# Optimization experiments

Hardware: AMD Instinct MI355X
Metric: run time of the kernel (lower is better)

The kernel has to match this reference:

```python
import jax, jax.numpy as jnp
import numpy as np

# footprints from the module: RB = 8-neighbor ring (center excluded), G = 4-neighbor cross
RB_OFFSETS = [(-1, -1), (-1, 0), (-1, 1), (0, -1), (0, 1), (1, -1), (1, 0), (1, 1)]
G_OFFSETS = [(-1, 0), (0, -1), (0, 1), (1, 0)]
N_ITER = 3


def _footprint_median(x, offsets):
    """scipy.ndimage.median_filter with a boolean footprint.
    scipy uses rank = n//2 of the sorted footprint values (no averaging for even n)
    and 'reflect' boundary mode (== numpy 'symmetric' padding).
    x: [B, H, W]
    """
    B, H, W = x.shape
    xp = jnp.pad(x, ((0, 0), (1, 1), (1, 1)), mode='symmetric')
    vals = jnp.stack([xp[:, 1 + dy:1 + dy + H, 1 + dx:1 + dx + W]
                      for dy, dx in offsets], axis=0)  # [n, B, H, W]
    n = len(offsets)
    return jnp.sort(vals, axis=0)[n // 2]


def _conv3(x, k):
    """3x3 conv with symmetric padding. x: [B,H,W], k: [3,3] -> [B,H,W]."""
    xp = jnp.pad(x, ((0, 0), (1, 1), (1, 1)), mode='symmetric')[:, None]  # [B,1,H+2,W+2]
    kern = k[None, None].astype(x.dtype)  # [1,1,3,3]
    out = jax.lax.conv_general_dilated(xp, kern, (1, 1), 'VALID')
    return out[:, 0]


def _demosaick(x):
    """Naive bilinear demosaick of a GRBG Bayer mosaic. x: [B,H,W] -> [B,3,H,W]."""
    B, H, W = x.shape
    yy, xx = jnp.meshgrid(jnp.arange(H), jnp.arange(W), indexing='ij')
    r_mask = ((yy % 2 == 0) & (xx % 2 == 1)).astype(x.dtype)
    b_mask = ((yy % 2 == 1) & (xx % 2 == 0)).astype(x.dtype)
    g_mask = 1.0 - r_mask - b_mask
    KG = jnp.array([[0., 1., 0.], [1., 4., 1.], [0., 1., 0.]]) / 4.0
    KRB = jnp.array([[1., 2., 1.], [2., 4., 2.], [1., 2., 1.]]) / 4.0
    R = _conv3(x * r_mask, KRB)
    G = _conv3(x * g_mask, KG)
    Bc = _conv3(x * b_mask, KRB)
    return jnp.stack([R, G, Bc], axis=1)


def reference(image):
    # image: [B, 1, H, W] Bayer mosaic
    d = _demosaick(image[:, 0])  # [B, 3, H, W]
    R, G, B = d[:, 0], d[:, 1], d[:, 2]
    for _ in range(N_ITER):
        # medians are non-differentiable in the original (numpy roundtrip)
        R = jax.lax.stop_gradient(_footprint_median(R - G, RB_OFFSETS)) + G
        B = jax.lax.stop_gradient(_footprint_median(B - G, RB_OFFSETS)) + G
        G = 0.5 * (jax.lax.stop_gradient(_footprint_median(G - R, G_OFFSETS))
                   + jax.lax.stop_gradient(_footprint_median(G - B, G_OFFSETS))
                   + R + B)
    return jnp.stack([R, G, B], axis=1)


def setup_inputs() -> dict:
    key = jax.random.key(0)
    image = jax.random.uniform(key, (8, 1, 1024, 1024), dtype=jnp.float32)
    return {"image": image}
```

## Files before the change

### kernel.cpp

```cpp
#include <hip/hip_runtime.h>

#define HH 1024
#define WW 1024
#define NB 8
constexpr int PLANE = HH * WW;

#define S   84
#define RG  46
#define NTHR 512

typedef _Float16 h2 __attribute__((ext_vector_type(2)));

__device__ __forceinline__ int clampi(int v, int lo, int hi) {
    return v < lo ? lo : (v > hi ? hi : v);
}

union U2H { unsigned u; h2 h; };
__device__ __forceinline__ h2 u2h(unsigned v) { U2H x; x.u = v; return x.h; }
__device__ __forceinline__ unsigned h2u(h2 h) { U2H x; x.h = h; return x.u; }
__device__ __forceinline__ unsigned packdiff(float a, float b) {
    h2 h; h.x = (_Float16)a; h.y = (_Float16)b; return h2u(h);
}

__device__ __forceinline__ void cswap2(h2& a, h2& b) {
    h2 lo = __builtin_elementwise_min(a, b);
    b = __builtin_elementwise_max(a, b);
    a = lo;
}

__device__ __forceinline__ h2 med8p(h2 v0, h2 v1, h2 v2, h2 v3,
                                    h2 v4, h2 v5, h2 v6, h2 v7) {
    cswap2(v0, v1); cswap2(v2, v3); cswap2(v4, v5); cswap2(v6, v7);
    cswap2(v0, v2); cswap2(v1, v3); cswap2(v4, v6); cswap2(v5, v7);
    cswap2(v1, v2); cswap2(v5, v6);
    h2 p2 = __builtin_elementwise_min(v2, v6), p3 = __builtin_elementwise_min(v3, v7);
    h2 p4 = __builtin_elementwise_max(v0, v4), p5 = __builtin_elementwise_max(v1, v5);
    return __builtin_elementwise_max(__builtin_elementwise_min(p3, p5),
                                     __builtin_elementwise_max(p2, p4));
}

__device__ __forceinline__ h2 med4p(h2 a, h2 b, h2 c, h2 d) {
    h2 ab_hi = __builtin_elementwise_max(a, b), ab_lo = __builtin_elementwise_min(a, b);
    h2 cd_hi = __builtin_elementwise_max(c, d), cd_lo = __builtin_elementwise_min(c, d);
    return __builtin_elementwise_max(__builtin_elementwise_min(ab_hi, cd_hi),
                                     __builtin_elementwise_max(ab_lo, cd_lo));
}

__device__ __forceinline__ void demo_acc(float v, int pyn, int pxn, int ady, int adx,
                                         float& accR, float& accG, float& accB) {
    bool isr = (pyn == 0) && (pxn == 1);
    bool isb = (pyn == 1) && (pxn == 0);
    float wrb = 0.25f * (float)((2 - ady) * (2 - adx));
    int man = ady + adx;
    float wg = (man == 0) ? 1.0f : ((man == 1) ? 0.25f : 0.0f);
    accR += isr ? wrb * v : 0.0f;
    accB += isb ? wrb * v : 0.0f;
    accG += (!isr && !isb) ? wg * v : 0.0f;
}

template <int CA>
__device__ __forceinline__ void load4u(const unsigned* row, int c0, unsigned w[4]) {
    if constexpr (CA == 0) {
        uint4 q = *reinterpret_cast<const uint4*>(row + c0);
        w[0] = q.x; w[1] = q.y; w[2] = q.z; w[3] = q.w;
    } else {
        uint2 a = *reinterpret_cast<const uint2*>(row + c0);
        uint2 b = *reinterpret_cast<const uint2*>(row + c0 + 2);
        w[0] = a.x; w[1] = a.y; w[2] = b.x; w[3] = b.y;
    }
}
template <int CA>
__device__ __forceinline__ void load6u(const unsigned* row, int c0, unsigned w[6]) {
    if constexpr (CA == 0) {
        uint4 q = *reinterpret_cast<const uint4*>(row + c0);
        w[0] = row[c0 - 1];
        w[1] = q.x; w[2] = q.y; w[3] = q.z; w[4] = q.w;
        w[5] = row[c0 + 4];
    } else {
        uint4 a = *reinterpret_cast<const uint4*>(row + c0 - 2);
        uint4 b = *reinterpret_cast<const uint4*>(row + c0 + 2);
        w[0] = a.y; w[1] = a.z; w[2] = a.w; w[3] = b.x; w[4] = b.y; w[5] = b.z;
    }
}
template <int CA>
__device__ __forceinline__ void store4u(unsigned* row, int c0, const unsigned v[4]) {
    if constexpr (CA == 0) {
        *reinterpret_cast<uint4*>(row + c0) = make_uint4(v[0], v[1], v[2], v[3]);
    } else {
        *reinterpret_cast<uint2*>(row + c0) = make_uint2(v[0], v[1]);
        *reinterpret_cast<uint2*>(row + c0 + 2) = make_uint2(v[2], v[3]);
    }
}
__device__ __forceinline__ void load4h(const _Float16* rowp, int c0, float g[4]) {
    h2 a = *reinterpret_cast<const h2*>(rowp + c0);
    h2 b = *reinterpret_cast<const h2*>(rowp + c0 + 2);
    g[0] = (float)a.x; g[1] = (float)a.y; g[2] = (float)b.x; g[3] = (float)b.y;
}
__device__ __forceinline__ void store4h(_Float16* rowp, int c0, const float v[4]) {
    h2 a; a.x = (_Float16)v[0]; a.y = (_Float16)v[1];
    h2 b; b.x = (_Float16)v[2]; b.y = (_Float16)v[3];
    *reinterpret_cast<h2*>(rowp + c0) = a;
    *reinterpret_cast<h2*>(rowp + c0 + 2) = b;
}

template <int R0, int NRP, int C0, int NG>
__device__ __forceinline__ void p1_int(const unsigned* __restrict__ sdRB,
                                       unsigned* __restrict__ uRB, int tid) {
    static_assert((C0 & 3) == 2, "p1_int needs C0 % 4 == 2");
    if (tid < NRP * NG) {
        int rp = tid / NG, g = tid - rp * NG;
        int r0 = R0 + 2 * rp;
        int c0 = C0 + 4 * g;
        int B = c0 - 2;
        unsigned w[4][6];
#pragma unroll
        for (int i = 0; i < 4; ++i) {
            const unsigned* row = &sdRB[(r0 - 1 + i) * S + B];
            uint4 q0 = *reinterpret_cast<const uint4*>(row);
            uint4 q1 = *reinterpret_cast<const uint4*>(row + 4);
            w[i][0] = q0.y; w[i][1] = q0.z; w[i][2] = q0.w;
            w[i][3] = q1.x; w[i][4] = q1.y; w[i][5] = q1.z;
        }
#pragma unroll
        for (int rr = 0; rr < 2; ++rr) {
            unsigned rv[4];
#pragma unroll
            for (int i = 0; i < 4; ++i) {
                h2 m = med8p(u2h(w[rr][i]), u2h(w[rr][i + 1]), u2h(w[rr][i + 2]),
                             u2h(w[rr + 1][i]), u2h(w[rr + 1][i + 2]),
                             u2h(w[rr + 2][i]), u2h(w[rr + 2][i + 1]), u2h(w[rr + 2][i + 2]));
                rv[i] = h2u(-m);
            }
            store4u<2>(&uRB[(r0 + rr) * S], c0, rv);
        }
    }
}

template <int R0, int NRP, int C0, int NG, int CA, bool FINAL>
__device__ __forceinline__ void p2_int(_Float16* __restrict__ sG, unsigned* __restrict__ sdRB,
                                       const unsigned* __restrict__ uRB, int tid,
                                       int y0, int x0,
                                       float* __restrict__ oR, float* __restrict__ oG,
                                       float* __restrict__ oB) {
    if (tid < NRP * NG) {
        int rp = tid / NG, g = tid - rp * NG;
        int r0 = R0 + 2 * rp;
        int c0 = C0 + 4 * g;
        unsigned wm[4], wp[4], w0[6], w1[6];
        load4u<CA>(&uRB[(r0 - 1) * S], c0, wm);
        load6u<CA>(&uRB[(r0) * S], c0, w0);
        load6u<CA>(&uRB[(r0 + 1) * S], c0, w1);
        load4u<CA>(&uRB[(r0 + 2) * S], c0, wp);
        float g0[4], g1[4];
        load4h(&sG[r0 * S], c0, g0);
        load4h(&sG[(r0 + 1) * S], c0, g1);
        float Rv[2][4], Gv[2][4], Bv[2][4];
#pragma unroll
        for (int i = 0; i < 4; ++i) {
            {
                h2 m = med4p(u2h(wm[i]), u2h(w0[i]), u2h(w0[i + 2]), u2h(w1[i + 1]));
                h2 uc = u2h(w0[i + 1]);
                float Gc = g0[i];
                float Rn = Gc - (float)uc.x, Bn = Gc - (float)uc.y;
                float Gn = 0.5f * ((float)m.x + (float)m.y + Rn + Bn);
                Rv[0][i] = Rn; Gv[0][i] = Gn; Bv[0][i] = Bn;
            }
            {
                h2 m = med4p(u2h(w0[i + 1]), u2h(w1[i]), u2h(w1[i + 2]), u2h(wp[i]));
                h2 uc = u2h(w1[i + 1]);
                float Gc = g1[i];
                float Rn = Gc - (float)uc.x, Bn = Gc - (float)uc.y;
                float Gn = 0.5f * ((float)m.x + (float)m.y + Rn + Bn);
                Rv[1][i] = Rn; Gv[1][i] = Gn; Bv[1][i] = Bn;
            }
        }
        if constexpr (FINAL) {
#pragma unroll
            for (int rr = 0; rr < 2; ++rr) {
                size_t o = (size_t)(y0 + r0 + rr) * WW + (x0 + c0);
                *reinterpret_cast<float4*>(&oR[o]) = make_float4(Rv[rr][0], Rv[rr][1], Rv[rr][2], Rv[rr][3]);
                *reinterpret_cast<float4*>(&oG[o]) = make_float4(Gv[rr][0], Gv[rr][1], Gv[rr][2], Gv[rr][3]);
                *reinterpret_cast<float4*>(&oB[o]) = make_float4(Bv[rr][0], Bv[rr][1], Bv[rr][2], Bv[rr][3]);
            }
        } else {
#pragma unroll
            for (int rr = 0; rr < 2; ++rr) {
                unsigned pd[4];
#pragma unroll
                for (int i = 0; i < 4; ++i)
                    pd[i] = packdiff(Rv[rr][i] - Gv[rr][i], Bv[rr][i] - Gv[rr][i]);
                store4h(&sG[(r0 + rr) * S], c0, Gv[rr]);
                store4u<CA>(&sdRB[(r0 + rr) * S], c0, pd);
            }
        }
    }
}

__device__ void p1_b(const unsigned* sdRB, unsigned* uRB, int tid,
                     int y0, int x0, int rlo, int nr, int clo, int nc) {
    for (int t = tid; t < nr * nc; t += NTHR) {
        int r = rlo + t / nc, c = clo + t - (t / nc) * nc;
        int gy = clampi(y0 + r, 0, HH - 1), gx = clampi(x0 + c, 0, WW - 1);
        int rm = clampi(gy - 1, 0, HH - 1) - y0, rp = clampi(gy + 1, 0, HH - 1) - y0;
        int cm = clampi(gx - 1, 0, WW - 1) - x0, cp = clampi(gx + 1, 0, WW - 1) - x0;
        h2 m = med8p(u2h(sdRB[rm * S + cm]), u2h(sdRB[rm * S + c]), u2h(sdRB[rm * S + cp]),
                     u2h(sdRB[r * S + cm]), u2h(sdRB[r * S + cp]),
                     u2h(sdRB[rp * S + cm]), u2h(sdRB[rp * S + c]), u2h(sdRB[rp * S + cp]));
        uRB[r * S + c] = h2u(-m);
    }
}

__device__ void p2_b(_Float16* sG, unsigned* sdRB, const unsigned* uRB, int tid,
                     int y0, int x0, int rlo, int nr, int clo, int nc, bool fin,
                     float* oR, float* oG, float* oB) {
    for (int t = tid; t < nr * nc; t += NTHR) {
        int r = rlo + t / nc, c = clo + t - (t / nc) * nc;
        int gy = clampi(y0 + r, 0, HH - 1), gx = clampi(x0 + c, 0, WW - 1);
        int rm = clampi(gy - 1, 0, HH - 1) - y0, rp = clampi(gy + 1, 0, HH - 1) - y0;
        int cm = clampi(gx - 1, 0, WW - 1) - x0, cp = clampi(gx + 1, 0, WW - 1) - x0;
        h2 m = med4p(u2h(uRB[rm * S + c]), u2h(uRB[r * S + cm]),
                     u2h(uRB[r * S + cp]), u2h(uRB[rp * S + c]));
        h2 uc = u2h(uRB[r * S + c]);
        float Gc = (float)sG[r * S + c];
        float Rn = Gc - (float)uc.x, Bn = Gc - (float)uc.y;
        float Gn = 0.5f * ((float)m.x + (float)m.y + Rn + Bn);
        if (fin) {
            size_t o = (size_t)(y0 + r) * WW + (x0 + c);
            oR[o] = Rn; oG[o] = Gn; oB[o] = Bn;
        } else {
            sG[r * S + c] = (_Float16)Gn;
            sdRB[r * S + c] = packdiff(Rn - Gn, Bn - Gn);
        }
    }
}

__global__ __launch_bounds__(512, 8) void fused_kernel(const float* __restrict__ img,
                                                       float* __restrict__ dst) {
    __shared__ __align__(16) unsigned smem[9660];
    unsigned* uRB = smem;
    unsigned* sdRB = smem + RG * S;
    _Float16* sG = reinterpret_cast<_Float16*>(smem + 2 * RG * S);
    float* sI = reinterpret_cast<float*>(smem);

    int bx = blockIdx.x, by = blockIdx.y, bb = blockIdx.z;
    int x0 = bx * 64 - 8, y0 = by * 32 - 7;
    const float* im = img + (size_t)bb * PLANE;
    float* oR = dst + (size_t)bb * 3 * PLANE;
    float* oG = oR + PLANE;
    float* oB = oR + 2 * PLANE;
    int tid = threadIdx.x;
    bool interior = (bx >= 1 && bx <= 14 && by >= 1 && by <= 30);

    if (interior) {
        for (int t = tid; t < RG * 20; t += NTHR) {
            int r = t / 20, k = t - (t / 20) * 20;
            *reinterpret_cast<float4*>(&sI[r * S + 4 * k]) =
                *reinterpret_cast<const float4*>(&im[(size_t)(y0 + r) * WW + x0 + 4 * k]);
        }
        __syncthreads();
        if (tid < 22 * 19) {
            int qi = tid / 19, g = tid - (tid / 19) * 19;
            int rA = 1 + 2 * qi;
            int B = 4 * g;
            float w[4][6];
#pragma unroll
            for (int i = 0; i < 4; ++i) {
                const float* row = &sI[(rA - 1 + i) * S + B];
                float4 a = *reinterpret_cast<const float4*>(row);
                float4 b = *reinterpret_cast<const float4*>(row + 4);
                w[i][0] = a.y; w[i][1] = a.z; w[i][2] = a.w;
                w[i][3] = b.x; w[i][4] = b.y; w[i][5] = b.z;
            }
#pragma unroll
            for (int q = 0; q < 2; ++q) {
                int jb = 1 + 2 * q;
                float g00 = w[1][jb];
                float r00 = 0.5f * (w[1][jb - 1] + w[1][jb + 1]);
                float b00 = 0.5f * (w[0][jb] + w[2][jb]);
                float r01 = w[1][jb + 1];
                float g01 = 0.25f * (w[0][jb + 1] + w[2][jb + 1] + w[1][jb] + w[1][jb + 2]);
                float b01 = 0.25f * (w[0][jb] + w[0][jb + 2] + w[2][jb] + w[2][jb + 2]);
                float b10 = w[2][jb];
                float g10 = 0.25f * (w[1][jb] + w[3][jb] + w[2][jb - 1] + w[2][jb + 1]);
                float r10 = 0.25f * (w[1][jb - 1] + w[1][jb + 1] + w[3][jb - 1] + w[3][jb + 1]);
                float g11 = w[2][jb + 1];
                float r11 = 0.5f * (w[1][jb + 1] + w[3][jb + 1]);
                float b11 = 0.5f * (w[2][jb] + w[2][jb + 2]);
                int a0 = rA * S + 2 + 4 * g + 2 * q;
                h2 gh0; gh0.x = (_Float16)g00; gh0.y = (_Float16)g01;
                h2 gh1; gh1.x = (_Float16)g10; gh1.y = (_Float16)g11;
                *reinterpret_cast<h2*>(&sG[a0]) = gh0;
                *reinterpret_cast<h2*>(&sG[a0 + S]) = gh1;
                *reinterpret_cast<uint2*>(&sdRB[a0]) =
                    make_uint2(packdiff(r00 - g00, b00 - g00), packdiff(r01 - g01, b01 - g01));
                *reinterpret_cast<uint2*>(&sdRB[a0 + S]) =
                    make_uint2(packdiff(r10 - g10, b10 - g10), packdiff(r11 - g11, b11 - g11));
            }
        }
        __syncthreads();
        p1_int<2, 21, 2, 19>(sdRB, uRB, tid);
        __syncthreads();
        p2_int<3, 20, 4, 18, 0, false>(sG, sdRB, uRB, tid, y0, x0, oR, oG, oB);
        __syncthreads();
        p1_int<4, 19, 2, 19>(sdRB, uRB, tid);
        __syncthreads();
        p2_int<5, 18, 6, 17, 2, false>(sG, sdRB, uRB, tid, y0, x0, oR, oG, oB);
        __syncthreads();
        p1_int<6, 17, 6, 17>(sdRB, uRB, tid);
        __syncthreads();
        p2_int<7, 16, 8, 16, 0, true>(sG, sdRB, uRB, tid, y0, x0, oR, oG, oB);
    } else {
        for (int t = tid; t < RG * S; t += NTHR) {
            int r = t / S, c = t - (t / S) * S;
            int gy = clampi(y0 + r, 0, HH - 1), gx = clampi(x0 + c, 0, WW - 1);
            sI[r * S + c] = im[(size_t)gy * WW + gx];
        }
        __syncthreads();
        {
            for (int t = tid; t < 44 * 76; t += NTHR) {
                int r = 1 + t / 76, c = 2 + t - (t / 76) * 76;
                int gy = clampi(y0 + r, 0, HH - 1), gx = clampi(x0 + c, 0, WW - 1);
                float accR = 0.f, accG = 0.f, accB = 0.f;
#pragma unroll
                for (int dy = -1; dy <= 1; ++dy)
#pragma unroll
                    for (int dx = -1; dx <= 1; ++dx) {
                        int cy = clampi(gy + dy, 0, HH - 1);
                        int cx = clampi(gx + dx, 0, WW - 1);
                        float v = sI[(cy - y0) * S + (cx - x0)];
                        demo_acc(v, cy & 1, cx & 1, dy < 0 ? -dy : dy, dx < 0 ? -dx : dx,
                                 accR, accG, accB);
                    }
                sG[r * S + c] = (_Float16)accG;
                sdRB[r * S + c] = packdiff(accR - accG, accB - accG);
            }
        }
        __syncthreads();
        p1_b(sdRB, uRB, tid, y0, x0, 2, 42, 3, 74);
        __syncthreads();
        p2_b(sG, sdRB, uRB, tid, y0, x0, 3, 40, 4, 72, false, oR, oG, oB);
        __syncthreads();
        p1_b(sdRB, uRB, tid, y0, x0, 4, 38, 5, 70);
        __syncthreads();
        p2_b(sG, sdRB, uRB, tid, y0, x0, 5, 36, 6, 68, false, oR, oG, oB);
        __syncthreads();
        p1_b(sdRB, uRB, tid, y0, x0, 6, 34, 7, 66);
        __syncthreads();
        p2_b(sG, sdRB, uRB, tid, y0, x0, 7, 32, 8, 64, true, oR, oG, oB);
    }
}

extern "C" void kernel_launch(void* const* d_in, const int* in_sizes, int n_in,
                              void* d_out, int out_size, void* d_ws, size_t ws_size,
                              hipStream_t stream) {
    const float* img = (const float*)d_in[0];
    float* out = (float*)d_out;
    dim3 block(NTHR);
    dim3 grid(16, 32, NB);
    fused_kernel<<<grid, block, 0, stream>>>(img, out);
}
```

Baseline: 137.5 us.

## Compute green update in packed fp16 and read input tile directly from global

The G update step in p2_int now stays in packed half2 arithmetic, using an alignbit lane swap to form the R+B and median sums, instead of converting to float and back. Interior blocks also drop the shared-memory staging of the raw input tile and its barrier, with each thread loading its 4x8 window straight from global memory. The aim is fewer conversion instructions, one less sync and fewer LDS round trips. In exchange, more arithmetic is done in fp16, which may add rounding error, and overlapping global reads are duplicated across threads, relying on the cache to absorb them.

Result: no change. 136.3 us (-0.9%).

```diff
diff --git a/kernel.cpp b/kernel.cpp
--- a/kernel.cpp
+++ b/kernel.cpp
@@ -20,6 +20,10 @@
 __device__ __forceinline__ unsigned h2u(h2 h) { U2H x; x.h = h; return x.u; }
 __device__ __forceinline__ unsigned packdiff(float a, float b) {
     h2 h; h.x = (_Float16)a; h.y = (_Float16)b; return h2u(h);
+}
+__device__ __forceinline__ h2 swap16(h2 x) {
+    unsigned u = h2u(x);
+    return u2h(__builtin_amdgcn_alignbit(u, u, 16));
 }
 
 __device__ __forceinline__ void cswap2(h2& a, h2& b) {
@@ -90,17 +94,6 @@
         *reinterpret_cast<uint2*>(row + c0) = make_uint2(v[0], v[1]);
         *reinterpret_cast<uint2*>(row + c0 + 2) = make_uint2(v[2], v[3]);
     }
-}
-__device__ __forceinline__ void load4h(const _Float16* rowp, int c0, float g[4]) {
-    h2 a = *reinterpret_cast<const h2*>(rowp + c0);
-    h2 b = *reinterpret_cast<const h2*>(rowp + c0 + 2);
-    g[0] = (float)a.x; g[1] = (float)a.y; g[2] = (float)b.x; g[3] = (float)b.y;
-}
-__device__ __forceinline__ void store4h(_Float16* rowp, int c0, const float v[4]) {
-    h2 a; a.x = (_Float16)v[0]; a.y = (_Float16)v[1];
-    h2 b; b.x = (_Float16)v[2]; b.y = (_Float16)v[3];
-    *reinterpret_cast<h2*>(rowp + c0) = a;
-    *reinterpret_cast<h2*>(rowp + c0 + 2) = b;
 }
 
 template <int R0, int NRP, int C0, int NG>
@@ -151,47 +144,64 @@
         load6u<CA>(&uRB[(r0) * S], c0, w0);
         load6u<CA>(&uRB[(r0 + 1) * S], c0, w1);
         load4u<CA>(&uRB[(r0 + 2) * S], c0, wp);
-        float g0[4], g1[4];
-        load4h(&sG[r0 * S], c0, g0);
-        load4h(&sG[(r0 + 1) * S], c0, g1);
-        float Rv[2][4], Gv[2][4], Bv[2][4];
+        h2 ga0 = *reinterpret_cast<const h2*>(&sG[r0 * S + c0]);
+        h2 ga1 = *reinterpret_cast<const h2*>(&sG[r0 * S + c0 + 2]);
+        h2 gb0 = *reinterpret_cast<const h2*>(&sG[(r0 + 1) * S + c0]);
+        h2 gb1 = *reinterpret_cast<const h2*>(&sG[(r0 + 1) * S + c0 + 2]);
+        _Float16 gr0[4] = {ga0.x, ga0.y, ga1.x, ga1.y};
+        _Float16 gr1[4] = {gb0.x, gb0.y, gb1.x, gb1.y};
+        const h2 half2v = {(_Float16)0.5f, (_Float16)0.5f};
+
+        unsigned nd0[4], nd1[4];
+        float R4[2][4], G4[2][4], B4[2][4];
 #pragma unroll
         for (int i = 0; i < 4; ++i) {
             {
                 h2 m = med4p(u2h(wm[i]), u2h(w0[i]), u2h(w0[i + 2]), u2h(w1[i + 1]));
                 h2 uc = u2h(w0[i + 1]);
-                float Gc = g0[i];
-                float Rn = Gc - (float)uc.x, Bn = Gc - (float)uc.y;
-                float Gn = 0.5f * ((float)m.x + (float)m.y + Rn + Bn);
-                Rv[0][i] = Rn; Gv[0][i] = Gn; Bv[0][i] = Bn;
+                h2 gg; gg.x = gr0[i]; gg.y = gr0[i];
+                h2 RB = gg - uc;
+                h2 Gn2 = ((m + swap16(m)) + (RB + swap16(RB))) * half2v;
+                if constexpr (FINAL) {
+                    R4[0][i] = (float)RB.x; B4[0][i] = (float)RB.y; G4[0][i] = (float)Gn2.x;
+                } else {
+                    nd0[i] = h2u(RB - Gn2);
+                    gr0[i] = Gn2.x;
+                }
             }
             {
                 h2 m = med4p(u2h(w0[i + 1]), u2h(w1[i]), u2h(w1[i + 2]), u2h(wp[i]));
                 h2 uc = u2h(w1[i + 1]);
-                float Gc = g1[i];
-                float Rn = Gc - (float)uc.x, Bn = Gc - (float)uc.y;
-                float Gn = 0.5f * ((float)m.x + (float)m.y + Rn + Bn);
-                Rv[1][i] = Rn; Gv[1][i] = Gn; Bv[1][i] = Bn;
+                h2 gg; gg.x = gr1[i]; gg.y = gr1[i];
+                h2 RB = gg - uc;
+                h2 Gn2 = ((m + swap16(m)) + (RB + swap16(RB))) * half2v;
+                if constexpr (FINAL) {
+                    R4[1][i] = (float)RB.x; B4[1][i] = (float)RB.y; G4[1][i] = (float)Gn2.x;
+                } else {
+                    nd1[i] = h2u(RB - Gn2);
+                    gr1[i] = Gn2.x;
+                }
             }
         }
         if constexpr (FINAL) {
 #pragma unroll
             for (int rr = 0; rr < 2; ++rr) {
                 size_t o = (size_t)(y0 + r0 + rr) * WW + (x0 + c0);
-                *reinterpret_cast<float4*>(&oR[o]) = make_float4(Rv[rr][0], Rv[rr][1], Rv[rr][2], Rv[rr][3]);
-                *reinterpret_cast<float4*>(&oG[o]) = make_float4(Gv[rr][0], Gv[rr][1], Gv[rr][2], Gv[rr][3]);
-                *reinterpret_cast<float4*>(&oB[o]) = make_float4(Bv[rr][0], Bv[rr][1], Bv[rr][2], Bv[rr][3]);
+                *reinterpret_cast<float4*>(&oR[o]) = make_float4(R4[rr][0], R4[rr][1], R4[rr][2], R4[rr][3]);
+                *reinterpret_cast<float4*>(&oG[o]) = make_float4(G4[rr][0], G4[rr][1], G4[rr][2], G4[rr][3]);
+                *reinterpret_cast<float4*>(&oB[o]) = make_float4(B4[rr][0], B4[rr][1], B4[rr][2], B4[rr][3]);
             }
         } else {
-#pragma unroll
-            for (int rr = 0; rr < 2; ++rr) {
-                unsigned pd[4];
-#pragma unroll
-                for (int i = 0; i < 4; ++i)
-                    pd[i] = packdiff(Rv[rr][i] - Gv[rr][i], Bv[rr][i] - Gv[rr][i]);
-                store4h(&sG[(r0 + rr) * S], c0, Gv[rr]);
-                store4u<CA>(&sdRB[(r0 + rr) * S], c0, pd);
-            }
+            h2 s00; s00.x = gr0[0]; s00.y = gr0[1];
+            h2 s01; s01.x = gr0[2]; s01.y = gr0[3];
+            h2 s10; s10.x = gr1[0]; s10.y = gr1[1];
+            h2 s11; s11.x = gr1[2]; s11.y = gr1[3];
+            *reinterpret_cast<h2*>(&sG[r0 * S + c0]) = s00;
+            *reinterpret_cast<h2*>(&sG[r0 * S + c0 + 2]) = s01;
+            *reinterpret_cast<h2*>(&sG[(r0 + 1) * S + c0]) = s10;
+            *reinterpret_cast<h2*>(&sG[(r0 + 1) * S + c0 + 2]) = s11;
+            store4u<CA>(&sdRB[r0 * S], c0, nd0);
+            store4u<CA>(&sdRB[(r0 + 1) * S], c0, nd1);
         }
     }
 }
@@ -252,22 +262,16 @@
     bool interior = (bx >= 1 && bx <= 14 && by >= 1 && by <= 30);
 
     if (interior) {
-        for (int t = tid; t < RG * 20; t += NTHR) {
-            int r = t / 20, k = t - (t / 20) * 20;
-            *reinterpret_cast<float4*>(&sI[r * S + 4 * k]) =
-                *reinterpret_cast<const float4*>(&im[(size_t)(y0 + r) * WW + x0 + 4 * k]);
-        }
-        __syncthreads();
         if (tid < 22 * 19) {
             int qi = tid / 19, g = tid - (tid / 19) * 19;
             int rA = 1 + 2 * qi;
             int B = 4 * g;
+            const float* base = im + (size_t)(y0 + rA - 1) * WW + (x0 + B);
             float w[4][6];
 #pragma unroll
             for (int i = 0; i < 4; ++i) {
-                const float* row = &sI[(rA - 1 + i) * S + B];
-                float4 a = *reinterpret_cast<const float4*>(row);
-                float4 b = *reinterpret_cast<const float4*>(row + 4);
+                float4 a = *reinterpret_cast<const float4*>(base + (size_t)i * WW);
+                float4 b = *reinterpret_cast<const float4*>(base + (size_t)i * WW + 4);
                 w[i][0] = a.y; w[i][1] = a.z; w[i][2] = a.w;
                 w[i][3] = b.x; w[i][4] = b.y; w[i][5] = b.z;
             }
```
